# Kernel tuning notes

Hardware: AMD Instinct MI355X
Metric: run time of the kernel (lower is better)

The kernel has to match this reference:

```python
import jax, jax.numpy as jnp
import numpy as np

N = 1_000_000
W = 20  # layer_width


def setup_inputs() -> dict:
    key = jax.random.key(0)
    ks = jax.random.split(key, 8)
    s = 0.5  # modest init scale for tanh net
    return {
        "t": jax.random.normal(ks[0], (N, 1), dtype=jnp.float32),
        "W1": jax.random.normal(ks[1], (1, W), dtype=jnp.float32) * s,
        "b1": jnp.zeros((W,), jnp.float32),
        "W2": jax.random.normal(ks[2], (W, W), dtype=jnp.float32) * s / np.sqrt(W),
        "b2": jnp.zeros((W,), jnp.float32),
        "W3": jax.random.normal(ks[3], (W, W), dtype=jnp.float32) * s / np.sqrt(W),
        "b3": jnp.zeros((W,), jnp.float32),
        "W4": jax.random.normal(ks[4], (W, W), dtype=jnp.float32) * s / np.sqrt(W),
        "b4": jnp.zeros((W,), jnp.float32),
        "Wo": jax.random.normal(ks[5], (W, 3), dtype=jnp.float32) * s / np.sqrt(W),
        "bo": jnp.zeros((3,), jnp.float32),
        "c1": jnp.float32(1.0),
        "c2": jnpp if False else jnp.float32(1.0),
        "c3": jnp.float32(1.0),
    }


def reference(t, W1, b1, W2, b2, W3, b3, W4, b4, Wo, bo, c1, c2, c3):
    # DenseBlock(4, 20): four tanh hidden layers + linear head to [x, y, z]
    def mlp(tt):
        h = jnp.tanh(tt @ W1 + b1)
        h = jnp.tanh(h @ W2 + b2)
        h = jnp.tanh(h @ W3 + b3)
        h = jnp.tanh(h @ W4 + b4)
        return h @ Wo + bo  # [N, 3]

    # forward-mode AD: one JVP pass gives d[x,y,z]/dt for every sample
    out, dout = jax.jvp(mlp, (t,), (jnp.ones_like(t),))
    x, y, z = out[:, 0:1], out[:, 1:2], out[:, 2:3]
    dx, dy, dz = dout[:, 0:1], dout[:, 1:2], dout[:, 2:3]
    # Lorenz residuals (log_opt=False -> vars used directly)
    fx = dx - c1 * (y - x)
    fy = dy - x * (c2 - z) + y
    fz = dz - x * y + c3 * z
    return jnp.concatenate([x, y, z, fx, fy, fz], axis=1)  # [N, 6]
```

## Files before the change

kernel.cpp:

```cpp
#include <hip/hip_runtime.h>

#define NBLK 256

__device__ __forceinline__ float fast_tanh(float x) {
    float e = __expf(2.0f * x);
    return 1.0f - 2.0f * __builtin_amdgcn_rcpf(e + 1.0f);
}

__global__ __launch_bounds__(NBLK) void pinn_kernel(
    const float* __restrict__ T,
    const float* __restrict__ W1, const float* __restrict__ b1,
    const float* __restrict__ W2, const float* __restrict__ b2,
    const float* __restrict__ W3, const float* __restrict__ b3,
    const float* __restrict__ W4, const float* __restrict__ b4,
    const float* __restrict__ Wo, const float* __restrict__ bo,
    const float* __restrict__ C1, const float* __restrict__ C2, const float* __restrict__ C3,
    float* __restrict__ out, int n)
{
    __shared__ __align__(16) float sW[1200];
    __shared__ __align__(16) float sB[64];
    __shared__ __align__(16) float sW1[20];
    __shared__ __align__(16) float sb1[20];
    __shared__ __align__(16) float sWoT[64];
    __shared__ float sbo[4];

    const int tid = threadIdx.x;
    for (int i2 = tid; i2 < 400; i2 += NBLK) {
        sW[i2]       = W2[i2];
        sW[400 + i2] = W3[i2];
        sW[800 + i2] = W4[i2];
    }
    if (tid < 20) {
        sW1[tid] = W1[tid];
        sb1[tid] = b1[tid];
        sB[tid]      = b2[tid];
        sB[20 + tid] = b3[tid];
        sB[40 + tid] = b4[tid];
    }
    if (tid < 60) sWoT[(tid % 3) * 20 + (tid / 3)] = Wo[tid];
    if (tid < 3)  sbo[tid] = bo[tid];
    __syncthreads();

    const int i = blockIdx.x * NBLK + tid;
    if (i >= n) return;

    const float t = T[i];

    float h[20], dh[20];

#pragma unroll
    for (int j = 0; j < 20; j += 4) {
        const float4 w = *reinterpret_cast<const float4*>(sW1 + j);
        const float4 b = *reinterpret_cast<const float4*>(sb1 + j);
        float zz[4] = { t * w.x + b.x, t * w.y + b.y, t * w.z + b.z, t * w.w + b.w };
        float dz[4] = { w.x, w.y, w.z, w.w };
#pragma unroll
        for (int q = 0; q < 4; ++q) {
            float e = fast_tanh(zz[q]);
            h[j + q]  = e;
            dh[j + q] = (1.0f - e * e) * dz[q];
        }
    }

#pragma unroll 1
    for (int L = 0; L < 3; ++L) {
        const float* __restrict__ w  = sW + L * 400;
        const float* __restrict__ bb = sB + L * 20;
        float nh[20], ndh[20];
#pragma unroll
        for (int j = 0; j < 20; j += 4) {
            float a0 = bb[j], a1 = bb[j + 1], a2 = bb[j + 2], a3 = bb[j + 3];
            float d0 = 0.f, d1 = 0.f, d2 = 0.f, d3 = 0.f;
#pragma unroll
            for (int k = 0; k < 20; ++k) {
                const float4 ww = *reinterpret_cast<const float4*>(w + k * 20 + j);
                const float hk = h[k], dk = dh[k];
                a0 += hk * ww.x; a1 += hk * ww.y; a2 += hk * ww.z; a3 += hk * ww.w;
                d0 += dk * ww.x; d1 += dk * ww.y; d2 += dk * ww.z; d3 += dk * ww.w;
            }
            float e0 = fast_tanh(a0), e1 = fast_tanh(a1), e2 = fast_tanh(a2), e3 = fast_tanh(a3);
            nh[j] = e0; nh[j + 1] = e1; nh[j + 2] = e2; nh[j + 3] = e3;
            ndh[j]     = (1.0f - e0 * e0) * d0;
            ndh[j + 1] = (1.0f - e1 * e1) * d1;
            ndh[j + 2] = (1.0f - e2 * e2) * d2;
            ndh[j + 3] = (1.0f - e3 * e3) * d3;
        }
#pragma unroll
        for (int j = 0; j < 20; ++j) { h[j] = nh[j]; dh[j] = ndh[j]; }
    }

    float o[3], dO[3];
#pragma unroll
    for (int j = 0; j < 3; ++j) {
        float a = sbo[j], d = 0.f;
#pragma unroll
        for (int k = 0; k < 20; k += 4) {
            const float4 ww = *reinterpret_cast<const float4*>(sWoT + j * 20 + k);
            a += h[k] * ww.x + h[k + 1] * ww.y + h[k + 2] * ww.z + h[k + 3] * ww.w;
            d += dh[k] * ww.x + dh[k + 1] * ww.y + dh[k + 2] * ww.z + dh[k + 3] * ww.w;
        }
        o[j] = a; dO[j] = d;
    }

    const float x = o[0], y = o[1], zz = o[2];
    const float dx = dO[0], dy = dO[1], dz = dO[2];
    const float c1 = C1[0], c2 = C2[0], c3 = C3[0];

    const float fx = dx - c1 * (y - x);
    const float fy = dy - x * (c2 - zz) + y;
    const float fz = dz - x * y + c3 * zz;

    float2* po = reinterpret_cast<float2*>(out + (size_t)i * 6);
    po[0] = make_float2(x,  y);
    po[1] = make_float2(zz, fx);
    po[2] = make_float2(fy, fz);
}

extern "C" void kernel_launch(void* const* d_in, const int* in_sizes, int n_in,
                              void* d_out, int out_size, void* d_ws, size_t ws_size,
                              hipStream_t stream) {
    const float* T  = (const float*)d_in[0];
    const float* W1 = (const float*)d_in[1];
    const float* b1 = (const float*)d_in[2];
    const float* W2 = (const float*)d_in[3];
    const float* b2 = (const float*)d_in[4];
    const float* W3 = (const float*)d_in[5];
    const float* b3 = (const float*)d_in[6];
    const float* W4 = (const float*)d_in[7];
    const float* b4 = (const float*)d_in[8];
    const float* Wo = (const float*)d_in[9];
    const float* bo = (const float*)d_in[10];
    const float* C1 = (const float*)d_in[11];
    const float* C2 = (const float*)d_in[12];
    const float* C3 = (const float*)d_in[13];
    float* out = (float*)d_out;

    const int n = in_sizes[0];
    const int blocks = (n + NBLK - 1) / NBLK;
    pinn_kernel<<<blocks, NBLK, 0, stream>>>(T, W1, b1, W2, b2, W3, b3, W4, b4,
                                             Wo, bo, C1, C2, C3, out, n);
}
```

Before: 178.2 us.

## Read weights as wave-uniform scalar loads instead of staging in LDS

Removes the shared-memory staging of all weights and the block barrier, and reads the weights straight from global memory with indices that are the same across the wave, so the compiler can turn them into scalar loads. The layer loops are reordered to an outer-product form over k, which keeps 40 accumulators live. Out-of-range threads are clamped rather than returned early, so the loads stay uniform. tanh now uses exp2 with a folded constant. The risks are scalar-cache pressure and higher register use.

```diff
diff --git a/kernel.cpp b/kernel.cpp
--- a/kernel.cpp
+++ b/kernel.cpp
@@ -3,7 +3,7 @@
 #define NBLK 256
 
 __device__ __forceinline__ float fast_tanh(float x) {
-    float e = __expf(2.0f * x);
+    float e = __builtin_amdgcn_exp2f(x * 2.88539008f);
     return 1.0f - 2.0f * __builtin_amdgcn_rcpf(e + 1.0f);
 }
 
@@ -17,103 +17,70 @@
     const float* __restrict__ C1, const float* __restrict__ C2, const float* __restrict__ C3,
     float* __restrict__ out, int n)
 {
-    __shared__ __align__(16) float sW[1200];
-    __shared__ __align__(16) float sB[64];
-    __shared__ __align__(16) float sW1[20];
-    __shared__ __align__(16) float sb1[20];
-    __shared__ __align__(16) float sWoT[64];
-    __shared__ float sbo[4];
-
-    const int tid = threadIdx.x;
-    for (int i2 = tid; i2 < 400; i2 += NBLK) {
-        sW[i2]       = W2[i2];
-        sW[400 + i2] = W3[i2];
-        sW[800 + i2] = W4[i2];
-    }
-    if (tid < 20) {
-        sW1[tid] = W1[tid];
-        sb1[tid] = b1[tid];
-        sB[tid]      = b2[tid];
-        sB[20 + tid] = b3[tid];
-        sB[40 + tid] = b4[tid];
-    }
-    if (tid < 60) sWoT[(tid % 3) * 20 + (tid / 3)] = Wo[tid];
-    if (tid < 3)  sbo[tid] = bo[tid];
-    __syncthreads();
-
-    const int i = blockIdx.x * NBLK + tid;
-    if (i >= n) return;
-
+    const int i0 = blockIdx.x * NBLK + threadIdx.x;
+    const int i  = (i0 < n) ? i0 : (n - 1);
     const float t = T[i];
 
-    float h[20], dh[20];
+    float h[20], d[20];
 
 #pragma unroll
-    for (int j = 0; j < 20; j += 4) {
-        const float4 w = *reinterpret_cast<const float4*>(sW1 + j);
-        const float4 b = *reinterpret_cast<const float4*>(sb1 + j);
-        float zz[4] = { t * w.x + b.x, t * w.y + b.y, t * w.z + b.z, t * w.w + b.w };
-        float dz[4] = { w.x, w.y, w.z, w.w };
-#pragma unroll
-        for (int q = 0; q < 4; ++q) {
-            float e = fast_tanh(zz[q]);
-            h[j + q]  = e;
-            dh[j + q] = (1.0f - e * e) * dz[q];
-        }
+    for (int j = 0; j < 20; ++j) {
+        const float w = W1[j];
+        const float e = fast_tanh(fmaf(t, w, b1[j]));
+        h[j] = e;
+        d[j] = (1.0f - e * e) * w;
     }
 
 #pragma unroll 1
     for (int L = 0; L < 3; ++L) {
-        const float* __restrict__ w  = sW + L * 400;
-        const float* __restrict__ bb = sB + L * 20;
-        float nh[20], ndh[20];
+        const float* __restrict__ WP = (L == 0) ? W2 : (L == 1) ? W3 : W4;
+        const float* __restrict__ BP = (L == 0) ? b2 : (L == 1) ? b3 : b4;
+        float a[20], dd[20];
 #pragma unroll
-        for (int j = 0; j < 20; j += 4) {
-            float a0 = bb[j], a1 = bb[j + 1], a2 = bb[j + 2], a3 = bb[j + 3];
-            float d0 = 0.f, d1 = 0.f, d2 = 0.f, d3 = 0.f;
+        for (int j = 0; j < 20; ++j) { a[j] = BP[j]; dd[j] = 0.0f; }
 #pragma unroll
-            for (int k = 0; k < 20; ++k) {
-                const float4 ww = *reinterpret_cast<const float4*>(w + k * 20 + j);
-                const float hk = h[k], dk = dh[k];
-                a0 += hk * ww.x; a1 += hk * ww.y; a2 += hk * ww.z; a3 += hk * ww.w;
-                d0 += dk * ww.x; d1 += dk * ww.y; d2 += dk * ww.z; d3 += dk * ww.w;
+        for (int k = 0; k < 20; ++k) {
+            const float hk = h[k], dk = d[k];
+#pragma unroll
+            for (int j = 0; j < 20; ++j) {
+                const float w = WP[k * 20 + j];
+                a[j]  = fmaf(hk, w, a[j]);
+                dd[j] = fmaf(dk, w, dd[j]);
             }
-            float e0 = fast_tanh(a0), e1 = fast_tanh(a1), e2 = fast_tanh(a2), e3 = fast_tanh(a3);
-            nh[j] = e0; nh[j + 1] = e1; nh[j + 2] = e2; nh[j + 3] = e3;
-            ndh[j]     = (1.0f - e0 * e0) * d0;
-            ndh[j + 1] = (1.0f - e1 * e1) * d1;
-            ndh[j + 2] = (1.0f - e2 * e2) * d2;
-            ndh[j + 3] = (1.0f - e3 * e3) * d3;
         }
 #pragma unroll
-        for (int j = 0; j < 20; ++j) { h[j] = nh[j]; dh[j] = ndh[j]; }
+        for (int j = 0; j < 20; ++j) {
+            const float e = fast_tanh(a[j]);
+            h[j] = e;
+            d[j] = (1.0f - e * e) * dd[j];
+        }
     }
 
-    float o[3], dO[3];
+    float o0 = bo[0], o1 = bo[1], o2 = bo[2];
+    float g0 = 0.0f, g1 = 0.0f, g2 = 0.0f;
 #pragma unroll
-    for (int j = 0; j < 3; ++j) {
-        float a = sbo[j], d = 0.f;
-#pragma unroll
-        for (int k = 0; k < 20; k += 4) {
-            const float4 ww = *reinterpret_cast<const float4*>(sWoT + j * 20 + k);
-            a += h[k] * ww.x + h[k + 1] * ww.y + h[k + 2] * ww.z + h[k + 3] * ww.w;
-            d += dh[k] * ww.x + dh[k + 1] * ww.y + dh[k + 2] * ww.z + dh[k + 3] * ww.w;
-        }
-        o[j] = a; dO[j] = d;
+    for (int k = 0; k < 20; ++k) {
+        const float hk = h[k], dk = d[k];
+        const float w0 = Wo[k * 3 + 0];
+        const float w1 = Wo[k * 3 + 1];
+        const float w2 = Wo[k * 3 + 2];
+        o0 = fmaf(hk, w0, o0);  g0 = fmaf(dk, w0, g0);
+        o1 = fmaf(hk, w1, o1);  g1 = fmaf(dk, w1, g1);
+        o2 = fmaf(hk, w2, o2);  g2 = fmaf(dk, w2, g2);
     }
 
-    const float x = o[0], y = o[1], zz = o[2];
-    const float dx = dO[0], dy = dO[1], dz = dO[2];
+    const float x = o0, y = o1, zz = o2;
     const float c1 = C1[0], c2 = C2[0], c3 = C3[0];
+    const float fx = g0 - c1 * (y - x);
+    const float fy = g1 - x * (c2 - zz) + y;
+    const float fz = g2 - x * y + c3 * zz;
 
-    const float fx = dx - c1 * (y - x);
-    const float fy = dy - x * (c2 - zz) + y;
-    const float fz = dz - x * y + c3 * zz;
-
-    float2* po = reinterpret_cast<float2*>(out + (size_t)i * 6);
-    po[0] = make_float2(x,  y);
-    po[1] = make_float2(zz, fx);
-    po[2] = make_float2(fy, fz);
+    if (i0 < n) {
+        float2* po = reinterpret_cast<float2*>(out + (size_t)i0 * 6);
+        po[0] = make_float2(x,  y);
+        po[1] = make_float2(zz, fx);
+        po[2] = make_float2(fy, fz);
+    }
 }
 
 extern "C" void kernel_launch(void* const* d_in, const int* in_sizes, int n_in,
```

New measurement: 162.9 us. -8.6%, faster.
